# Performance work log

Hardware: AMD Instinct MI355X
Metric: run time of the kernel (lower is better)

Reference implementation:

```python
import jax, jax.numpy as jnp
import numpy as np

WINDOW_SIZE = 11
SIGMA = 1.5
C1 = 0.01 ** 2
C2 = 0.03 ** 2


def _gaussian_window(window_size, sigma, channel, dtype=jnp.float32):
    x = np.arange(window_size) - window_size // 2
    g = np.exp(-(x.astype(np.float64) ** 2) / (2.0 * sigma ** 2))
    g = (g / g.sum()).astype(np.float32)
    w2d = np.outer(g, g)  # [K, K]
    # depthwise kernel: [C, 1, K, K] (OIHW with feature_group_count=C)
    w = np.broadcast_to(w2d, (channel, 1, window_size, window_size))
    return jnp.asarray(w, dtype=dtype)


def _dw_conv(x, window):
    # x: [B, C, H, W]; window: [C, 1, K, K]; SAME padding via pad=K//2 (K odd)
    k = window.shape[-1]
    p = k // 2
    return jax.lax.conv_general_dilated(
        x, window,
        window_strides=(1, 1),
        padding=((p, p), (p, p)),
        dimension_numbers=("NCHW", "OIHW", "NCHW"),
        feature_group_count=x.shape[1],
    )


def setup_inputs() -> dict:
    key = jax.random.key(0)
    k1, k2 = jax.random.split(key)
    shape = (32, 3, 512, 512)
    img1 = jax.random.uniform(k1, shape, dtype=jnp.float32)
    img2 = jax.random.uniform(k2, shape, dtype=jnp.float32)
    return {"img1": img1, "img2": img2}


def reference(img1, img2):
    channel = img1.shape[1]
    window = _gaussian_window(WINDOW_SIZE, SIGMA, channel, img1.dtype)

    mu1 = _dw_conv(img1, window)
    mu2 = _dw_conv(img2, window)
    mu1_sq = mu1 * mu1
    mu2_sq = mu2 * mu2
    mu1_mu2 = mu1 * mu2

    sigma1_sq = _dw_conv(img1 * img1, window) - mu1_sq
    sigma2_sq = _dw_conv(img2 * img2, window) - mu2_sq
    sigma12 = _dw_conv(img1 * img2, window) - mu1_mu2

    ssim_map = ((2.0 * mu1_mu2 + C1) * (2.0 * sigma12 + C2)) / (
        (mu1_sq + mu2_sq + C1) * (sigma1_sq + sigma2_sq + C2)
    )
    return 1.0 - jnp.mean(ssim_map)
```

## Files before the change

kernel.cpp:

```cpp
#include <hip/hip_runtime.h>

#define HH 512
#define WW 512
#define PLANES 96
#define RSTRIP 32
#define NPIX 25165824.0f

#define G0 0.2660117f
#define G1 0.2130056f
#define G2 0.1093607f
#define G3 0.0360008f
#define G4 0.0075988f
#define G5 0.0010284f

#define C1F 1e-4f
#define C2F 9e-4f

typedef float v2f __attribute__((ext_vector_type(2)));
#define PKFMA(a, b, c) __builtin_elementwise_fma(a, b, c)

#define DECL_HIST2(Z) v2f Z##0={0,0},Z##1={0,0},Z##2={0,0},Z##3={0,0},Z##4={0,0},\
                          Z##5={0,0},Z##6={0,0},Z##7={0,0},Z##8={0,0},Z##9={0,0},Z##10={0,0}
#define SHIFT_HIST(Z) do{Z##0=Z##1;Z##1=Z##2;Z##2=Z##3;Z##3=Z##4;Z##4=Z##5;\
                         Z##5=Z##6;Z##6=Z##7;Z##7=Z##8;Z##8=Z##9;Z##9=Z##10;}while(0)
#define VCONV2(Z) PKFMA(g5, Z##0+Z##10, PKFMA(g4, Z##1+Z##9, PKFMA(g3, Z##2+Z##8,\
                  PKFMA(g2, Z##3+Z##7, PKFMA(g1, Z##4+Z##6, g0*Z##5)))))

__global__ __launch_bounds__(256) __attribute__((amdgpu_waves_per_eu(6, 8)))
void ssim_main(const float* __restrict__ img1,
               const float* __restrict__ img2,
               float* __restrict__ acc) {
    __shared__ v2f luv[2][4][80];
    const int tid  = threadIdx.x;
    const int lane = tid & 63;
    const int wv   = tid >> 6;
    const int base = blockIdx.x * 256 + wv * 64;
    const int r0   = blockIdx.y * RSTRIP;
    const int p    = blockIdx.z;
    const size_t pb = (size_t)p * (HH * WW);

    const int cs = base - 5 + lane;
    const bool in_main = (unsigned)cs < (unsigned)WW;
    const bool halo    = lane < 10;
    const bool in_halo = halo && (unsigned)(cs + 64) < (unsigned)WW;

    const float* rx = img1 + pb + (ptrdiff_t)(r0 - 5) * WW + cs;
    const float* ry = img2 + pb + (ptrdiff_t)(r0 - 5) * WW + cs;

    const v2f g0 = {G0, G0}, g1 = {G1, G1}, g2 = {G2, G2},
              g3 = {G3, G3}, g4 = {G4, G4}, g5 = {G5, G5};

    DECL_HIST2(AB); DECL_HIST2(PQ);

    float cx = 0.f, cy = 0.f, chx = 0.f, chy = 0.f;
    if ((unsigned)(r0 - 5) < (unsigned)HH) {
        if (in_main) { cx  = rx[0];  cy  = ry[0];  }
        if (in_halo) { chx = rx[64]; chy = ry[64]; }
    }

    float lsum = 0.f;
    const int tend = r0 + RSTRIP + 4;

#pragma unroll 6
    for (int t = r0 - 5; t <= tend; ++t, rx += WW, ry += WW) {
        SHIFT_HIST(AB); SHIFT_HIST(PQ);

        float nx2 = 0.f, ny2 = 0.f, nhx = 0.f, nhy = 0.f;
        const int tn = t + 1;
        if (tn <= tend && (unsigned)tn < (unsigned)HH) {
            if (in_main) { nx2 = rx[WW];      ny2 = ry[WW];      }
            if (in_halo) { nhx = rx[WW + 64]; nhy = ry[WW + 64]; }
        }

        v2f nAB = {0.f, 0.f}, nPQ = {0.f, 0.f};
        if ((unsigned)t < (unsigned)HH) {
            v2f* sb = &luv[t & 1][wv][0];
            sb[lane] = v2f{cx + cy, cx - cy};
            if (halo) sb[64 + lane] = v2f{chx + chy, chx - chy};
            __asm__ volatile("" ::: "memory");
            __builtin_amdgcn_wave_barrier();

            const v2f* wp = sb + lane;
            {
                const v2f uv5 = wp[5];
                nAB = g0 * uv5;
                nPQ = g0 * (uv5 * uv5);
            }
#define HPAIR(KL, KR, GK) { \
            const v2f l = wp[KL], r = wp[KR]; \
            nAB = PKFMA(GK, l + r, nAB); \
            nPQ = PKFMA(GK, PKFMA(l, l, r * r), nPQ); }
            HPAIR(4, 6, g1) HPAIR(3, 7, g2) HPAIR(2, 8, g3)
            HPAIR(1, 9, g4) HPAIR(0, 10, g5)
#undef HPAIR
            __asm__ volatile("" ::: "memory");
            __builtin_amdgcn_wave_barrier();
        }
        cx = nx2; cy = ny2; chx = nhx; chy = nhy;
        AB10 = nAB; PQ10 = nPQ;

        const int s = t - 5 - r0;
        if ((unsigned)s < (unsigned)RSTRIP) {
            const v2f mu = VCONV2(AB);
            const v2f c2 = VCONV2(PQ);
            const float a = mu.x * mu.x;
            const float b = mu.y * mu.y;
            const float musq = 0.5f  * (a + b);
            const float mu12 = 0.25f * (a - b);
            const float csq  = 0.5f  * (c2.x + c2.y);
            const float cxy  = 0.25f * (c2.x - c2.y);
            const float ssum = csq - musq;
            const float s12  = cxy - mu12;
            const float num = fmaf(2.f, mu12, C1F) * fmaf(2.f, s12, C2F);
            const float den = (musq + C1F) * (ssum + C2F);
            lsum += num * __builtin_amdgcn_rcpf(den);
        }
    }

#pragma unroll
    for (int off = 32; off > 0; off >>= 1)
        lsum += __shfl_down(lsum, off, 64);
    __shared__ float ws4[4];
    if (lane == 0) ws4[wv] = lsum;
    __syncthreads();
    if (threadIdx.x == 0)
        atomicAdd(acc, ws4[0] + ws4[1] + ws4[2] + ws4[3]);
}

__global__ void ssim_zero(float* acc) { acc[0] = 0.f; }

__global__ void ssim_finalize(const float* __restrict__ acc, float* __restrict__ out) {
    out[0] = 1.f - acc[0] * (1.f / NPIX);
}

extern "C" void kernel_launch(void* const* d_in, const int* in_sizes, int n_in,
                              void* d_out, int out_size, void* d_ws, size_t ws_size,
                              hipStream_t stream) {
    const float* img1 = (const float*)d_in[0];
    const float* img2 = (const float*)d_in[1];
    float* out = (float*)d_out;
    float* acc = (float*)d_ws;

    ssim_zero<<<1, 1, 0, stream>>>(acc);
    dim3 grid(WW / 256, HH / RSTRIP, PLANES);
    ssim_main<<<grid, 256, 0, stream>>>(img1, img2, acc);
    ssim_finalize<<<1, 1, 0, stream>>>(acc, out);
}
```

Baseline: 273.4 us.

## Process two columns per thread with float2 loads and shared horizontal window

Each thread now handles two adjacent columns, loading float2 per row and keeping separate vertical histories for the even and odd column. A single 128-wide strip per wave is staged in one LDS buffer, and the 12 taps loaded from it serve both horizontal convolutions. This halves the grid to one block per row-strip and plane and lowers halo overhead per output. The cost is roughly double the register pressure, reflected in the relaxed waves-per-EU hint, plus fewer blocks and less occupancy. The double-buffered LDS row was also dropped in favour of a single buffer guarded by wave barriers.

Result: faster. 257.2 us (-5.9%).

```diff
diff --git a/kernel.cpp b/kernel.cpp
--- a/kernel.cpp
+++ b/kernel.cpp
@@ -26,94 +26,114 @@
 #define VCONV2(Z) PKFMA(g5, Z##0+Z##10, PKFMA(g4, Z##1+Z##9, PKFMA(g3, Z##2+Z##8,\
                   PKFMA(g2, Z##3+Z##7, PKFMA(g1, Z##4+Z##6, g0*Z##5)))))
 
-__global__ __launch_bounds__(256) __attribute__((amdgpu_waves_per_eu(6, 8)))
+#define HCONV(T0,T1,T2,T3,T4,T5,T6,T7,T8,T9,T10, NAB, NPQ) do { \
+    NAB = g0 * (T5);            NPQ = g0 * ((T5) * (T5)); \
+    NAB = PKFMA(g1, (T4)+(T6),  NAB); NPQ = PKFMA(g1, PKFMA((T4),(T4),(T6)*(T6)),   NPQ); \
+    NAB = PKFMA(g2, (T3)+(T7),  NAB); NPQ = PKFMA(g2, PKFMA((T3),(T3),(T7)*(T7)),   NPQ); \
+    NAB = PKFMA(g3, (T2)+(T8),  NAB); NPQ = PKFMA(g3, PKFMA((T2),(T2),(T8)*(T8)),   NPQ); \
+    NAB = PKFMA(g4, (T1)+(T9),  NAB); NPQ = PKFMA(g4, PKFMA((T1),(T1),(T9)*(T9)),   NPQ); \
+    NAB = PKFMA(g5, (T0)+(T10), NAB); NPQ = PKFMA(g5, PKFMA((T0),(T0),(T10)*(T10)), NPQ); \
+} while (0)
+
+#define EPILOG(ZAB, ZPQ) do { \
+    const v2f mu = VCONV2(ZAB); \
+    const v2f c2 = VCONV2(ZPQ); \
+    const float a = mu.x * mu.x; \
+    const float b = mu.y * mu.y; \
+    const float musq = 0.5f  * (a + b);        \
+    const float mu12 = 0.25f * (a - b);        \
+    const float csq  = 0.5f  * (c2.x + c2.y);  \
+    const float cxy  = 0.25f * (c2.x - c2.y);  \
+    const float ssum = csq - musq; \
+    const float s12  = cxy - mu12; \
+    const float num = fmaf(2.f, mu12, C1F) * fmaf(2.f, s12, C2F); \
+    const float den = (musq + C1F) * (ssum + C2F); \
+    lsum += num * __builtin_amdgcn_rcpf(den); \
+} while (0)
+
+__global__ __launch_bounds__(256) __attribute__((amdgpu_waves_per_eu(3, 8)))
 void ssim_main(const float* __restrict__ img1,
                const float* __restrict__ img2,
                float* __restrict__ acc) {
-    __shared__ v2f luv[2][4][80];
+    __shared__ __align__(16) v2f luv[4][144];
     const int tid  = threadIdx.x;
     const int lane = tid & 63;
     const int wv   = tid >> 6;
-    const int base = blockIdx.x * 256 + wv * 64;
+    const int base = wv * 128;
     const int r0   = blockIdx.y * RSTRIP;
     const int p    = blockIdx.z;
     const size_t pb = (size_t)p * (HH * WW);
+    const int c0   = base + 2 * lane;
 
-    const int cs = base - 5 + lane;
-    const bool in_main = (unsigned)cs < (unsigned)WW;
-    const bool halo    = lane < 10;
-    const bool in_halo = halo && (unsigned)(cs + 64) < (unsigned)WW;
+    const bool hl = (lane < 5);
+    const bool hhalo = (lane < 12);
+    int hcol = hl ? (base - 5 + lane) : (base + 123 + lane);
+    const bool hv = hhalo && ((unsigned)hcol < (unsigned)WW);
+    if (!hv) hcol = 0;
+    const int hslot = hl ? lane : (128 + lane);
 
-    const float* rx = img1 + pb + (ptrdiff_t)(r0 - 5) * WW + cs;
-    const float* ry = img2 + pb + (ptrdiff_t)(r0 - 5) * WW + cs;
+    const float* rx = img1 + pb + (ptrdiff_t)(r0 - 5) * WW + c0;
+    const float* ry = img2 + pb + (ptrdiff_t)(r0 - 5) * WW + c0;
+    const float* hx = img1 + pb + (ptrdiff_t)(r0 - 5) * WW + hcol;
+    const float* hy = img2 + pb + (ptrdiff_t)(r0 - 5) * WW + hcol;
 
     const v2f g0 = {G0, G0}, g1 = {G1, G1}, g2 = {G2, G2},
               g3 = {G3, G3}, g4 = {G4, G4}, g5 = {G5, G5};
 
-    DECL_HIST2(AB); DECL_HIST2(PQ);
+    DECL_HIST2(ABe); DECL_HIST2(PQe);
+    DECL_HIST2(ABo); DECL_HIST2(PQo);
 
-    float cx = 0.f, cy = 0.f, chx = 0.f, chy = 0.f;
+    v2f cxv = {0.f, 0.f}, cyv = {0.f, 0.f};
+    float chx = 0.f, chy = 0.f;
     if ((unsigned)(r0 - 5) < (unsigned)HH) {
-        if (in_main) { cx  = rx[0];  cy  = ry[0];  }
-        if (in_halo) { chx = rx[64]; chy = ry[64]; }
+        __builtin_memcpy(&cxv, rx, 8);
+        __builtin_memcpy(&cyv, ry, 8);
+        if (hv) { chx = hx[0]; chy = hy[0]; }
     }
 
+    v2f* const sb = &luv[wv][0];
     float lsum = 0.f;
     const int tend = r0 + RSTRIP + 4;
 
 #pragma unroll 6
-    for (int t = r0 - 5; t <= tend; ++t, rx += WW, ry += WW) {
-        SHIFT_HIST(AB); SHIFT_HIST(PQ);
+    for (int t = r0 - 5; t <= tend; ++t, rx += WW, ry += WW, hx += WW, hy += WW) {
+        SHIFT_HIST(ABe); SHIFT_HIST(PQe); SHIFT_HIST(ABo); SHIFT_HIST(PQo);
 
-        float nx2 = 0.f, ny2 = 0.f, nhx = 0.f, nhy = 0.f;
+        v2f nxv = {0.f, 0.f}, nyv = {0.f, 0.f};
+        float nhx = 0.f, nhy = 0.f;
         const int tn = t + 1;
         if (tn <= tend && (unsigned)tn < (unsigned)HH) {
-            if (in_main) { nx2 = rx[WW];      ny2 = ry[WW];      }
-            if (in_halo) { nhx = rx[WW + 64]; nhy = ry[WW + 64]; }
+            __builtin_memcpy(&nxv, rx + WW, 8);
+            __builtin_memcpy(&nyv, ry + WW, 8);
+            if (hv) { nhx = hx[WW]; nhy = hy[WW]; }
         }
 
-        v2f nAB = {0.f, 0.f}, nPQ = {0.f, 0.f};
+        v2f nABe = {0,0}, nPQe = {0,0}, nABo = {0,0}, nPQo = {0,0};
         if ((unsigned)t < (unsigned)HH) {
-            v2f* sb = &luv[t & 1][wv][0];
-            sb[lane] = v2f{cx + cy, cx - cy};
-            if (halo) sb[64 + lane] = v2f{chx + chy, chx - chy};
+            const v2f u2 = cxv + cyv;
+            const v2f w2 = cxv - cyv;
+            sb[2 * lane + 5] = v2f{u2.x, w2.x};
+            sb[2 * lane + 6] = v2f{u2.y, w2.y};
+            if (hhalo) sb[hslot] = v2f{chx + chy, chx - chy};
             __asm__ volatile("" ::: "memory");
             __builtin_amdgcn_wave_barrier();
 
-            const v2f* wp = sb + lane;
-            {
-                const v2f uv5 = wp[5];
-                nAB = g0 * uv5;
-                nPQ = g0 * (uv5 * uv5);
-            }
-#define HPAIR(KL, KR, GK) { \
-            const v2f l = wp[KL], r = wp[KR]; \
-            nAB = PKFMA(GK, l + r, nAB); \
-            nPQ = PKFMA(GK, PKFMA(l, l, r * r), nPQ); }
-            HPAIR(4, 6, g1) HPAIR(3, 7, g2) HPAIR(2, 8, g3)
-            HPAIR(1, 9, g4) HPAIR(0, 10, g5)
-#undef HPAIR
+            const v2f* wp = sb + 2 * lane;
+            const v2f t0 = wp[0], t1 = wp[1], t2 = wp[2],  t3 = wp[3];
+            const v2f t4 = wp[4], t5 = wp[5], t6 = wp[6],  t7 = wp[7];
+            const v2f t8 = wp[8], t9 = wp[9], ta = wp[10], tb = wp[11];
+            HCONV(t0,t1,t2,t3,t4,t5,t6,t7,t8,t9,ta, nABe, nPQe);
+            HCONV(t1,t2,t3,t4,t5,t6,t7,t8,t9,ta,tb, nABo, nPQo);
             __asm__ volatile("" ::: "memory");
             __builtin_amdgcn_wave_barrier();
         }
-        cx = nx2; cy = ny2; chx = nhx; chy = nhy;
-        AB10 = nAB; PQ10 = nPQ;
+        cxv = nxv; cyv = nyv; chx = nhx; chy = nhy;
+        ABe10 = nABe; PQe10 = nPQe; ABo10 = nABo; PQo10 = nPQo;
 
         const int s = t - 5 - r0;
         if ((unsigned)s < (unsigned)RSTRIP) {
-            const v2f mu = VCONV2(AB);
-            const v2f c2 = VCONV2(PQ);
-            const float a = mu.x * mu.x;
-            const float b = mu.y * mu.y;
-            const float musq = 0.5f  * (a + b);
-            const float mu12 = 0.25f * (a - b);
-            const float csq  = 0.5f  * (c2.x + c2.y);
-            const float cxy  = 0.25f * (c2.x - c2.y);
-            const float ssum = csq - musq;
-            const float s12  = cxy - mu12;
-            const float num = fmaf(2.f, mu12, C1F) * fmaf(2.f, s12, C2F);
-            const float den = (musq + C1F) * (ssum + C2F);
-            lsum += num * __builtin_amdgcn_rcpf(den);
+            EPILOG(ABe, PQe);
+            EPILOG(ABo, PQo);
         }
     }
 
@@ -142,7 +162,7 @@
     float* acc = (float*)d_ws;
 
     ssim_zero<<<1, 1, 0, stream>>>(acc);
-    dim3 grid(WW / 256, HH / RSTRIP, PLANES);
+    dim3 grid(1, HH / RSTRIP, PLANES);
     ssim_main<<<grid, 256, 0, stream>>>(img1, img2, acc);
     ssim_finalize<<<1, 1, 0, stream>>>(acc, out);
 }
```

## Split u/v planes in LDS, pair adjacent columns per lane, double row strip

Applied to the files above, without the earlier changes.

The horizontal pass is reorganized so each lane pair splits the u=x+y and v=x-y planes, and each lane computes two adjacent output columns packed in a v2f from separate float LDS arrays. Shuffles then exchange the results so each lane recovers its own u and v. The row strip per block grows from 32 to 64 to cut the 10-row vertical halo overhead, and the waves_per_eu minimum is relaxed to 4. The LDS buffer is no longer double-buffered, and the extra shuffles plus lane selects add ALU work.

Result: slower. 303.8 us (+11.2%).

```diff
diff --git a/kernel.cpp b/kernel.cpp
--- a/kernel.cpp
+++ b/kernel.cpp
@@ -3,7 +3,7 @@
 #define HH 512
 #define WW 512
 #define PLANES 96
-#define RSTRIP 32
+#define RSTRIP 64
 #define NPIX 25165824.0f
 
 #define G0 0.2660117f
@@ -26,11 +26,20 @@
 #define VCONV2(Z) PKFMA(g5, Z##0+Z##10, PKFMA(g4, Z##1+Z##9, PKFMA(g3, Z##2+Z##8,\
                   PKFMA(g2, Z##3+Z##7, PKFMA(g1, Z##4+Z##6, g0*Z##5)))))
 
-__global__ __launch_bounds__(256) __attribute__((amdgpu_waves_per_eu(6, 8)))
+#define HCONV(T0,T1,T2,T3,T4,T5,T6,T7,T8,T9,T10, NAB, NPQ) do { \
+    NAB = g0 * (T5);            NPQ = g0 * ((T5) * (T5)); \
+    NAB = PKFMA(g1, (T4)+(T6),  NAB); NPQ = PKFMA(g1, PKFMA((T4),(T4),(T6)*(T6)),   NPQ); \
+    NAB = PKFMA(g2, (T3)+(T7),  NAB); NPQ = PKFMA(g2, PKFMA((T3),(T3),(T7)*(T7)),   NPQ); \
+    NAB = PKFMA(g3, (T2)+(T8),  NAB); NPQ = PKFMA(g3, PKFMA((T2),(T2),(T8)*(T8)),   NPQ); \
+    NAB = PKFMA(g4, (T1)+(T9),  NAB); NPQ = PKFMA(g4, PKFMA((T1),(T1),(T9)*(T9)),   NPQ); \
+    NAB = PKFMA(g5, (T0)+(T10), NAB); NPQ = PKFMA(g5, PKFMA((T0),(T0),(T10)*(T10)), NPQ); \
+} while (0)
+
+__global__ __launch_bounds__(256) __attribute__((amdgpu_waves_per_eu(4, 8)))
 void ssim_main(const float* __restrict__ img1,
                const float* __restrict__ img2,
                float* __restrict__ acc) {
-    __shared__ v2f luv[2][4][80];
+    __shared__ float pl[4][150];
     const int tid  = threadIdx.x;
     const int lane = tid & 63;
     const int wv   = tid >> 6;
@@ -40,9 +49,13 @@
     const size_t pb = (size_t)p * (HH * WW);
 
     const int cs = base - 5 + lane;
-    const bool in_main = (unsigned)cs < (unsigned)WW;
-    const bool halo    = lane < 10;
-    const bool in_halo = halo && (unsigned)(cs + 64) < (unsigned)WW;
+    const bool vmain = (unsigned)cs < (unsigned)WW;
+    const bool hh    = lane < 10;
+    const bool vhalo = hh && (unsigned)(cs + 64) < (unsigned)WW;
+
+    const int tau   = lane >> 1;
+    const int alpha = lane & 1;
+    const float* const wp = &pl[wv][alpha ? 75 : 0] + 2 * tau;
 
     const float* rx = img1 + pb + (ptrdiff_t)(r0 - 5) * WW + cs;
     const float* ry = img2 + pb + (ptrdiff_t)(r0 - 5) * WW + cs;
@@ -50,12 +63,12 @@
     const v2f g0 = {G0, G0}, g1 = {G1, G1}, g2 = {G2, G2},
               g3 = {G3, G3}, g4 = {G4, G4}, g5 = {G5, G5};
 
-    DECL_HIST2(AB); DECL_HIST2(PQ);
+    DECL_HIST2(SS); DECL_HIST2(QQ);
 
     float cx = 0.f, cy = 0.f, chx = 0.f, chy = 0.f;
     if ((unsigned)(r0 - 5) < (unsigned)HH) {
-        if (in_main) { cx  = rx[0];  cy  = ry[0];  }
-        if (in_halo) { chx = rx[64]; chy = ry[64]; }
+        if (vmain) { cx  = rx[0];  cy  = ry[0];  }
+        if (vhalo) { chx = rx[64]; chy = ry[64]; }
     }
 
     float lsum = 0.f;
@@ -63,52 +76,56 @@
 
 #pragma unroll 6
     for (int t = r0 - 5; t <= tend; ++t, rx += WW, ry += WW) {
-        SHIFT_HIST(AB); SHIFT_HIST(PQ);
+        SHIFT_HIST(SS); SHIFT_HIST(QQ);
 
-        float nx2 = 0.f, ny2 = 0.f, nhx = 0.f, nhy = 0.f;
+        float nx = 0.f, ny = 0.f, nhx = 0.f, nhy = 0.f;
         const int tn = t + 1;
         if (tn <= tend && (unsigned)tn < (unsigned)HH) {
-            if (in_main) { nx2 = rx[WW];      ny2 = ry[WW];      }
-            if (in_halo) { nhx = rx[WW + 64]; nhy = ry[WW + 64]; }
+            if (vmain) { nx  = rx[WW];      ny  = ry[WW];      }
+            if (vhalo) { nhx = rx[WW + 64]; nhy = ry[WW + 64]; }
         }
 
-        v2f nAB = {0.f, 0.f}, nPQ = {0.f, 0.f};
+        v2f nS = {0.f, 0.f}, nQ = {0.f, 0.f};
         if ((unsigned)t < (unsigned)HH) {
-            v2f* sb = &luv[t & 1][wv][0];
-            sb[lane] = v2f{cx + cy, cx - cy};
-            if (halo) sb[64 + lane] = v2f{chx + chy, chx - chy};
+            float* const up = &pl[wv][0];
+            up[lane]      = cx + cy;
+            up[75 + lane] = cx - cy;
+            if (hh) { up[64 + lane]  = chx + chy;
+                      up[139 + lane] = chx - chy; }
             __asm__ volatile("" ::: "memory");
             __builtin_amdgcn_wave_barrier();
 
-            const v2f* wp = sb + lane;
-            {
-                const v2f uv5 = wp[5];
-                nAB = g0 * uv5;
-                nPQ = g0 * (uv5 * uv5);
-            }
-#define HPAIR(KL, KR, GK) { \
-            const v2f l = wp[KL], r = wp[KR]; \
-            nAB = PKFMA(GK, l + r, nAB); \
-            nPQ = PKFMA(GK, PKFMA(l, l, r * r), nPQ); }
-            HPAIR(4, 6, g1) HPAIR(3, 7, g2) HPAIR(2, 8, g3)
-            HPAIR(1, 9, g4) HPAIR(0, 10, g5)
-#undef HPAIR
+            const float u0 = wp[0], u1 = wp[1], u2 = wp[2],  u3 = wp[3];
+            const float u4 = wp[4], u5 = wp[5], u6 = wp[6],  u7 = wp[7];
+            const float u8 = wp[8], u9 = wp[9], uA = wp[10], uB = wp[11];
+            const v2f T0 = {u0, u1}, T1 = {u1, u2}, T2 = {u2, u3}, T3 = {u3, u4};
+            const v2f T4 = {u4, u5}, T5 = {u5, u6}, T6 = {u6, u7}, T7 = {u7, u8};
+            const v2f T8 = {u8, u9}, T9 = {u9, uA}, TA = {uA, uB};
+            HCONV(T0,T1,T2,T3,T4,T5,T6,T7,T8,T9,TA, nS, nQ);
             __asm__ volatile("" ::: "memory");
             __builtin_amdgcn_wave_barrier();
         }
-        cx = nx2; cy = ny2; chx = nhx; chy = nhy;
-        AB10 = nAB; PQ10 = nPQ;
+        cx = nx; cy = ny; chx = nhx; chy = nhy;
+        SS10 = nS; QQ10 = nQ;
 
         const int s = t - 5 - r0;
         if ((unsigned)s < (unsigned)RSTRIP) {
-            const v2f mu = VCONV2(AB);
-            const v2f c2 = VCONV2(PQ);
-            const float a = mu.x * mu.x;
-            const float b = mu.y * mu.y;
+            const v2f mu = VCONV2(SS);
+            const v2f c2 = VCONV2(QQ);
+            const float smu = alpha ? mu.x : mu.y;
+            const float sc2 = alpha ? c2.x : c2.y;
+            const float rmu = __shfl_xor(smu, 1, 64);
+            const float rc2 = __shfl_xor(sc2, 1, 64);
+            const float mu_u = alpha ? rmu  : mu.x;
+            const float mu_v = alpha ? mu.y : rmu;
+            const float cu2  = alpha ? rc2  : c2.x;
+            const float cv2  = alpha ? c2.y : rc2;
+            const float a = mu_u * mu_u;
+            const float b = mu_v * mu_v;
             const float musq = 0.5f  * (a + b);
             const float mu12 = 0.25f * (a - b);
-            const float csq  = 0.5f  * (c2.x + c2.y);
-            const float cxy  = 0.25f * (c2.x - c2.y);
+            const float csq  = 0.5f  * (cu2 + cv2);
+            const float cxy  = 0.25f * (cu2 - cv2);
             const float ssum = csq - musq;
             const float s12  = cxy - mu12;
             const float num = fmaf(2.f, mu12, C1F) * fmaf(2.f, s12, C2F);
```
